# Kernel tuning notes

Hardware: AMD Instinct MI355X
Metric: run time of the kernel (lower is better)

## Reference

```python
import jax, jax.numpy as jnp
import numpy as np

N_NODES = 20000
N_EDGES = 100000
N_SNAP = 2
N_DIM, E_DIM, OUT_DIM, HEADS = 64, 32, 64, 2


def edge_gat(x, ef, src, dst, Wn, We, al, ar, ae, b):
    # DGL EdgeGATConv: fc (no bias), edge-aware attention, edge softmax over
    # incoming edges, message = (ft_src + ft_edge) * alpha, final additive bias.
    H, D = al.shape
    ft = (x @ Wn).reshape(-1, H, D)                # [N,H,D]
    fe = (ef @ We).reshape(-1, H, D)               # [E,H,D]
    el = jnp.einsum('nhd,hd->nh', ft, al)          # [N,H]
    er = jnp.einsum('nhd,hd->nh', ft, ar)          # [N,H]
    ee = jnp.einsum('ehd,hd->eh', fe, ae)          # [E,H]
    logits = jax.nn.leaky_relu(el[src] + er[dst] + ee, 0.2)  # [E,H]
    m = jax.ops.segment_max(logits, dst, num_segments=N_NODES)
    p = jnp.exp(logits - m[dst])
    s = jax.ops.segment_sum(p, dst, num_segments=N_NODES)
    a = p / s[dst]                                 # edge softmax per dst node
    msg = (ft[src] + fe) * a[..., None]            # [E,H,D]
    return jax.ops.segment_sum(msg, dst, num_segments=N_NODES) + b  # [N,H,D]


def gnn_rnn(x, ef, src, dst, params):
    # GNN_RNN.forward per snapshot: stacked EdgeGAT layers, head-mean each.
    for (Wn, We, al, ar, ae, b) in params:
        x = edge_gat(x, ef, src, dst, Wn, We, al, ar, ae, b).mean(axis=1)
    return x


def _mk_layer(key, in_d, e_d, out_d, heads, scale=0.1):
    ks = jax.random.split(key, 6)
    return dict(
        Wn=jax.random.normal(ks[0], (in_d, heads * out_d), jnp.float32) * scale,
        We=jax.random.normal(ks[1], (e_d, heads * out_d), jnp.float32) * scale,
        al=jax.random.normal(ks[2], (heads, out_d), jnp.float32) * scale,
        ar=jax.random.normal(ks[3], (heads, out_d), jnp.float32) * scale,
        ae=jax.random.normal(ks[4], (heads, out_d), jnp.float32) * scale,
        b=jax.random.normal(ks[5], (heads, out_d), jnp.float32) * scale,
    )


def setup_inputs() -> dict:
    key = jax.random.key(0)
    ks = jax.random.split(key, 10)
    inp = {
        'x': jax.random.normal(ks[0], (N_SNAP, N_NODES, N_DIM), jnp.float32),
        'e': jax.random.normal(ks[1], (N_SNAP, N_EDGES, E_DIM), jnp.float32),
        'src': jax.random.randint(ks[2], (N_SNAP, N_EDGES), 0, N_NODES),
        'dst': jax.random.randint(ks[3], (N_SNAP, N_EDGES), 0, N_NODES),
    }
    enc0 = _mk_layer(ks[4], N_DIM, E_DIM, OUT_DIM, HEADS)
    enc1 = _mk_layer(ks[5], OUT_DIM, E_DIM, OUT_DIM, HEADS)
    dec0 = _mk_layer(ks[6], OUT_DIM, E_DIM, N_DIM, HEADS)
    dec1 = _mk_layer(ks[7], N_DIM, E_DIM, N_DIM, HEADS)
    for pref, lp in [('enc0', enc0), ('enc1', enc1), ('dec0', dec0), ('dec1', dec1)]:
        for k, v in lp.items():
            inp[f'{pref}_{k}'] = v
    inp['W_e2d'] = jax.random.normal(ks[8], (OUT_DIM, OUT_DIM), jnp.float32) * 0.1
    return inp


def reference(x, e, src, dst,
              enc0_Wn, enc0_We, enc0_al, enc0_ar, enc0_ae, enc0_b,
              enc1_Wn, enc1_We, enc1_al, enc1_ar, enc1_ae, enc1_b,
              W_e2d,
              dec0_Wn, dec0_We, dec0_al, dec0_ar, dec0_ae, dec0_b,
              dec1_Wn, dec1_We, dec1_al, dec1_ar, dec1_ae, dec1_b):
    enc_params = [(enc0_Wn, enc0_We, enc0_al, enc0_ar, enc0_ae, enc0_b),
                  (enc1_Wn, enc1_We, enc1_al, enc1_ar, enc1_ae, enc1_b)]
    dec_params = [(dec0_Wn, dec0_We, dec0_al, dec0_ar, dec0_ae, dec0_b),
                  (dec1_Wn, dec1_We, dec1_al, dec1_ar, dec1_ae, dec1_b)]

    def per_snapshot(xs, es, ss, ds):
        h = gnn_rnn(xs, es, ss, ds, enc_params)   # encoder, [N,out_dim]
        h = h @ W_e2d.T                           # encoder_to_decoder (no bias)
        return gnn_rnn(h, es, ss, ds, dec_params) # decoder, [N,n_dim]

    decoded = jax.vmap(per_snapshot)(x, e, src, dst)  # [S,N,n_dim]
    return decoded[-1]
```

## Files before the change

kernel.cpp:

```cpp
#include <hip/hip_runtime.h>
#include <math.h>

#define N_NODES 20000
#define N_EDGES 100000

__device__ __forceinline__ float rl_f(float v, int l) {
    return __uint_as_float(__builtin_amdgcn_readlane(__float_as_uint(v), l));
}
__device__ __forceinline__ int rl_i(int v, int l) {
    return __builtin_amdgcn_readlane(v, l);
}
__device__ __forceinline__ float lrelu(float x) { return x > 0.f ? x : 0.2f * x; }

__global__ __launch_bounds__(256) void count_kernel(const int* __restrict__ dst,
                                                    int* __restrict__ cnt,
                                                    int* __restrict__ pos) {
    int e = blockIdx.x * 256 + threadIdx.x;
    if (e < N_EDGES) pos[e] = atomicAdd(&cnt[dst[e]], 1);
}

__global__ __launch_bounds__(256) void scanA_kernel(const int* __restrict__ cnt,
                                                    int* __restrict__ bsum) {
    __shared__ int wsum[4];
    const int tid = threadIdx.x;
    int idx = blockIdx.x * 256 + tid;
    int v = (idx < N_NODES) ? cnt[idx] : 0;
    int s = v;
#pragma unroll
    for (int off = 32; off; off >>= 1) s += __shfl_xor(s, off);
    if ((tid & 63) == 0) wsum[tid >> 6] = s;
    __syncthreads();
    if (tid == 0) bsum[blockIdx.x] = wsum[0] + wsum[1] + wsum[2] + wsum[3];
}

__global__ __launch_bounds__(256) void scanC_kernel(const int* __restrict__ cnt,
                                                    const int* __restrict__ bsum,
                                                    int* __restrict__ row_ptr) {
    __shared__ int sdata[256];
    __shared__ int s_boff;
    const int tid = threadIdx.x;
    const int b = blockIdx.x;
    int idx = b * 256 + tid;
    int v = (idx < N_NODES) ? cnt[idx] : 0;
    sdata[tid] = v;
    if (tid < 64) {
        int a = (tid < b) ? bsum[tid] : 0;
        if (64 + tid < b) a += bsum[64 + tid];
#pragma unroll
        for (int off = 32; off; off >>= 1) a += __shfl_xor(a, off);
        if (tid == 0) s_boff = a;
    }
    __syncthreads();
    for (int off = 1; off < 256; off <<= 1) {
        int t_ = (tid >= off) ? sdata[tid - off] : 0;
        __syncthreads();
        sdata[tid] += t_;
        __syncthreads();
    }
    if (idx < N_NODES) row_ptr[idx] = s_boff + sdata[tid] - v;
    if (b == 0 && tid == 0) row_ptr[N_NODES] = N_EDGES;
}

__global__ __launch_bounds__(256) void permE_kernel(const float* __restrict__ Efeat,
                                                    const int* __restrict__ src,
                                                    const int* __restrict__ dst,
                                                    const int* __restrict__ pos,
                                                    const int* __restrict__ row_ptr,
                                                    float* __restrict__ E_csr,
                                                    int* __restrict__ src_csr) {
    int idx = blockIdx.x * 256 + threadIdx.x;
    int e = idx >> 5, c = idx & 31;
    if (e >= N_EDGES) return;
    int j = row_ptr[dst[e]] + pos[e];
    E_csr[(size_t)j * 32 + c] = Efeat[(size_t)e * 32 + c];
    if (c == 0) src_csr[j] = src[e];
}

__global__ __launch_bounds__(256) void q_kernel(const float* __restrict__ We0, const float* __restrict__ ae0,
                                                const float* __restrict__ We1, const float* __restrict__ ae1,
                                                const float* __restrict__ We2, const float* __restrict__ ae2,
                                                const float* __restrict__ We3, const float* __restrict__ ae3,
                                                float* __restrict__ Q) {
    const int t = threadIdx.x;
    const int k = t >> 3, o = t & 7, L = o >> 1, h = o & 1;
    const float* We = (L == 0) ? We0 : (L == 1) ? We1 : (L == 2) ? We2 : We3;
    const float* ae = (L == 0) ? ae0 : (L == 1) ? ae1 : (L == 2) ? ae2 : ae3;
    float acc = 0.f;
#pragma unroll 8
    for (int d = 0; d < 64; d++) acc = fmaf(We[k * 128 + h * 64 + d], ae[h * 64 + d], acc);
    Q[t] = acc;
}

__global__ __launch_bounds__(256) void ee_kernel(const float* __restrict__ Efeat,
                                                 const int* __restrict__ dst,
                                                 const int* __restrict__ pos,
                                                 const int* __restrict__ row_ptr,
                                                 const float* __restrict__ Q,
                                                 float* __restrict__ EE_csr) {
    __shared__ float QS[256];
    const int tid = threadIdx.x;
    QS[tid] = Q[tid];
    __syncthreads();
    const int e = blockIdx.x * 32 + (tid >> 3);
    const int o = tid & 7;
    if (e >= N_EDGES) return;
    const int j = row_ptr[dst[e]] + pos[e];
    const float4* E4 = (const float4*)(Efeat + (size_t)e * 32);
    float acc = 0.f;
#pragma unroll
    for (int k4 = 0; k4 < 8; k4++) {
        float4 v = E4[k4];
        acc = fmaf(v.x, QS[(k4 * 4 + 0) * 8 + o], acc);
        acc = fmaf(v.y, QS[(k4 * 4 + 1) * 8 + o], acc);
        acc = fmaf(v.z, QS[(k4 * 4 + 2) * 8 + o], acc);
        acc = fmaf(v.w, QS[(k4 * 4 + 3) * 8 + o], acc);
    }
    EE_csr[(size_t)(o >> 1) * 2 * N_EDGES + (size_t)j * 2 + (o & 1)] = acc;
}

__global__ __launch_bounds__(256) void comb_kernel(const float* __restrict__ W_e2d,
                                                   const float* __restrict__ Wn,
                                                   float* __restrict__ Wcomb) {
    int idx = blockIdx.x * 256 + threadIdx.x;
    int j = idx >> 7, c = idx & 127;
    float acc = 0.f;
#pragma unroll 8
    for (int i = 0; i < 64; i++) acc = fmaf(W_e2d[i * 64 + j], Wn[i * 128 + c], acc);
    Wcomb[idx] = acc;
}

__global__ __launch_bounds__(256) void p4_kernel(const float* __restrict__ Wn0, const float* __restrict__ al0, const float* __restrict__ ar0,
                                                 const float* __restrict__ Wn1, const float* __restrict__ al1, const float* __restrict__ ar1,
                                                 const float* __restrict__ Wn2, const float* __restrict__ al2, const float* __restrict__ ar2,
                                                 const float* __restrict__ Wn3, const float* __restrict__ al3, const float* __restrict__ ar3,
                                                 float* __restrict__ P4) {
    const int L = blockIdx.x;
    const float* Wn = (L == 0) ? Wn0 : (L == 1) ? Wn1 : (L == 2) ? Wn2 : Wn3;
    const float* al = (L == 0) ? al0 : (L == 1) ? al1 : (L == 2) ? al2 : al3;
    const float* ar = (L == 0) ? ar0 : (L == 1) ? ar1 : (L == 2) ? ar2 : ar3;
    const int t = threadIdx.x;
    const int k = t >> 2, o = t & 3;
    const float* a = (o & 2) ? ar : al;
    const int h = o & 1;
    float acc = 0.f;
#pragma unroll 8
    for (int d = 0; d < 64; d++) acc = fmaf(Wn[k * 128 + h * 64 + d], a[h * 64 + d], acc);
    P4[L * 256 + t] = acc;
}

__global__ __launch_bounds__(256) void elr_kernel(const float* __restrict__ X,
                                                  const float* __restrict__ P4,
                                                  float2* __restrict__ EL2,
                                                  float2* __restrict__ ER2) {
    const int tid = threadIdx.x;
    const int lane = tid & 63;
    const int wave = tid >> 6;
    const float4 p = ((const float4*)P4)[lane];
    for (int node = blockIdx.x * 4 + wave; node < N_NODES; node += gridDim.x * 4) {
        float xv = X[node * 64 + lane];
        float e0 = xv * p.x, e1 = xv * p.y, f0 = xv * p.z, f1 = xv * p.w;
#pragma unroll
        for (int off = 32; off; off >>= 1) {
            e0 += __shfl_xor(e0, off);
            e1 += __shfl_xor(e1, off);
            f0 += __shfl_xor(f0, off);
            f1 += __shfl_xor(f1, off);
        }
        if (lane == 0) {
            EL2[node] = make_float2(e0, e1);
            ER2[node] = make_float2(f0, f1);
        }
    }
}

__global__ __launch_bounds__(256) void gather_kernel(const float* __restrict__ X,
                                                     const float2* __restrict__ EL2,
                                                     const float2* __restrict__ ER2,
                                                     const float* __restrict__ E_csr,
                                                     const int* __restrict__ src_csr,
                                                     const int* __restrict__ row_ptr,
                                                     const float2* __restrict__ EE_L,
                                                     float2* __restrict__ AX2,
                                                     float* __restrict__ AE) {
    const int tid = threadIdx.x;
    const int lane = tid & 63;
    const int node = blockIdx.x * 4 + (tid >> 6);
    if (node >= N_NODES) return;
    const float NEG_INF = -__builtin_inff();

    const int beg = row_ptr[node], end = row_ptr[node + 1];
    const int deg = end - beg;
    const float2 er = ER2[node];
    float l0 = 0.f, l1 = 0.f, aX0 = 0.f, aX1 = 0.f, aE = 0.f;

    if (deg <= 64) {
        int sn = 0;
        float lg0 = NEG_INF, lg1 = NEG_INF;
        if (lane < deg) {
            sn = src_csr[beg + lane];
            float2 ee = EE_L[beg + lane];
            float2 el = EL2[sn];
            lg0 = lrelu(el.x + er.x + ee.x);
            lg1 = lrelu(el.y + er.y + ee.y);
        }
        float m0 = lg0, m1 = lg1;
#pragma unroll
        for (int off = 32; off; off >>= 1) {
            m0 = fmaxf(m0, __shfl_xor(m0, off));
            m1 = fmaxf(m1, __shfl_xor(m1, off));
        }
        float w0 = (lane < deg) ? __expf(lg0 - m0) : 0.f;
        float w1 = (lane < deg) ? __expf(lg1 - m1) : 0.f;
        l0 = w0;
        l1 = w1;
#pragma unroll
        for (int off = 32; off; off >>= 1) {
            l0 += __shfl_xor(l0, off);
            l1 += __shfl_xor(l1, off);
        }
        int t = 0;
        for (; t + 4 <= deg; t += 4) {
            int s0 = rl_i(sn, t), s1 = rl_i(sn, t + 1);
            int s2 = rl_i(sn, t + 2), s3 = rl_i(sn, t + 3);
            float x0 = X[s0 * 64 + lane];
            float x1 = X[s1 * 64 + lane];
            float x2 = X[s2 * 64 + lane];
            float x3 = X[s3 * 64 + lane];
            const float* Eb = E_csr + (size_t)(beg + t) * 32 + (lane & 31);
            float e0 = Eb[0], e1 = Eb[32], e2 = Eb[64], e3 = Eb[96];
            float w00 = rl_f(w0, t), w01 = rl_f(w0, t + 1);
            float w02 = rl_f(w0, t + 2), w03 = rl_f(w0, t + 3);
            float w10 = rl_f(w1, t), w11 = rl_f(w1, t + 1);
            float w12 = rl_f(w1, t + 2), w13 = rl_f(w1, t + 3);
            aX0 = fmaf(w00, x0, aX0); aX1 = fmaf(w10, x0, aX1);
            aX0 = fmaf(w01, x1, aX0); aX1 = fmaf(w11, x1, aX1);
            aX0 = fmaf(w02, x2, aX0); aX1 = fmaf(w12, x2, aX1);
            aX0 = fmaf(w03, x3, aX0); aX1 = fmaf(w13, x3, aX1);
            aE = fmaf(lane < 32 ? w00 : w10, e0, aE);
            aE = fmaf(lane < 32 ? w01 : w11, e1, aE);
            aE = fmaf(lane < 32 ? w02 : w12, e2, aE);
            aE = fmaf(lane < 32 ? w03 : w13, e3, aE);
        }
        for (; t < deg; t++) {
            int st = rl_i(sn, t);
            float w0t = rl_f(w0, t), w1t = rl_f(w1, t);
            float xv = X[st * 64 + lane];
            float ev = E_csr[(size_t)(beg + t) * 32 + (lane & 31)];
            aX0 = fmaf(w0t, xv, aX0);
            aX1 = fmaf(w1t, xv, aX1);
            aE = fmaf(lane < 32 ? w0t : w1t, ev, aE);
        }
    } else {
        float m0 = NEG_INF, m1 = NEG_INF;
        for (int c = beg; c < end; c += 64) {
            int j = c + lane;
            float lg0 = NEG_INF, lg1 = NEG_INF;
            if (j < end) {
                int sn_ = src_csr[j];
                float2 ee = EE_L[j];
                float2 el = EL2[sn_];
                lg0 = lrelu(el.x + er.x + ee.x);
                lg1 = lrelu(el.y + er.y + ee.y);
            }
#pragma unroll
            for (int off = 32; off; off >>= 1) {
                lg0 = fmaxf(lg0, __shfl_xor(lg0, off));
                lg1 = fmaxf(lg1, __shfl_xor(lg1, off));
            }
            m0 = fmaxf(m0, lg0);
            m1 = fmaxf(m1, lg1);
        }
        for (int c = beg; c < end; c += 64) {
            int j = c + lane;
            int sn_ = 0;
            float lg0 = NEG_INF, lg1 = NEG_INF;
            if (j < end) {
                sn_ = src_csr[j];
                float2 ee = EE_L[j];
                float2 el = EL2[sn_];
                lg0 = lrelu(el.x + er.x + ee.x);
                lg1 = lrelu(el.y + er.y + ee.y);
            }
            float w0c = (j < end) ? __expf(lg0 - m0) : 0.f;
            float w1c = (j < end) ? __expf(lg1 - m1) : 0.f;
            float s0 = w0c, s1 = w1c;
#pragma unroll
            for (int off = 32; off; off >>= 1) {
                s0 += __shfl_xor(s0, off);
                s1 += __shfl_xor(s1, off);
            }
            l0 += s0;
            l1 += s1;
            int nch = (end - c) < 64 ? (end - c) : 64;
            for (int t = 0; t < nch; t++) {
                int st = rl_i(sn_, t);
                float w0t = rl_f(w0c, t), w1t = rl_f(w1c, t);
                float xv = X[st * 64 + lane];
                float ev = E_csr[(size_t)(c + t) * 32 + (lane & 31)];
                aX0 = fmaf(w0t, xv, aX0);
                aX1 = fmaf(w1t, xv, aX1);
                aE = fmaf(lane < 32 ? w0t : w1t, ev, aE);
            }
        }
    }
    const float inv0 = l0 > 0.f ? 1.f / l0 : 0.f;
    const float inv1 = l1 > 0.f ? 1.f / l1 : 0.f;
    AX2[node * 64 + lane] = make_float2(aX0 * inv0, aX1 * inv1);
    AE[node * 64 + lane] = aE * (lane < 32 ? inv0 : inv1);
}

__global__ __launch_bounds__(256) void epilogue_kernel(const float2* __restrict__ AX2,
                                                       const float* __restrict__ AE,
                                                       const float* __restrict__ Wn,
                                                       const float* __restrict__ We,
                                                       const float* __restrict__ bias,
                                                       const float* __restrict__ P4next,
                                                       const int has_next,
                                                       float* __restrict__ OUT,
                                                       float2* __restrict__ EL2,
                                                       float2* __restrict__ ER2) {
    __shared__ float4 WnS4[32 * 64];
    __shared__ float4 WeS4[16 * 64];
    const int tid = threadIdx.x;
    for (int idx = tid; idx < 32 * 64; idx += 256) {
        int k2 = idx >> 6, l = idx & 63;
        WnS4[idx] = make_float4(Wn[(2 * k2) * 128 + l], Wn[(2 * k2) * 128 + 64 + l],
                                Wn[(2 * k2 + 1) * 128 + l], Wn[(2 * k2 + 1) * 128 + 64 + l]);
    }
    for (int idx = tid; idx < 16 * 64; idx += 256) {
        int k2 = idx >> 6, l = idx & 63;
        WeS4[idx] = make_float4(We[(2 * k2) * 128 + l], We[(2 * k2) * 128 + 64 + l],
                                We[(2 * k2 + 1) * 128 + l], We[(2 * k2 + 1) * 128 + 64 + l]);
    }
    __syncthreads();
    const int lane = tid & 63;
    const int wave = tid >> 6;
    const float b0 = bias[lane], b1 = bias[64 + lane];
    const float4 p = has_next ? ((const float4*)P4next)[lane] : make_float4(0.f, 0.f, 0.f, 0.f);

    for (int base = blockIdx.x * 8 + wave * 2; base < N_NODES; base += gridDim.x * 8) {
        const int n0 = base, n1 = base + 1;
        float2 axa = AX2[n0 * 64 + lane];
        float2 axb = AX2[n1 * 64 + lane];
        float aea = AE[n0 * 64 + lane];
        float aeb = AE[n1 * 64 + lane];
        float r0a = 0.f, r1a = 0.f, r0b = 0.f, r1b = 0.f;
#pragma unroll
        for (int k2 = 0; k2 < 32; k2++) {
            float4 w4 = WnS4[k2 * 64 + lane];
            float a00 = rl_f(axa.x, 2 * k2), a01 = rl_f(axa.x, 2 * k2 + 1);
            float a10 = rl_f(axa.y, 2 * k2), a11 = rl_f(axa.y, 2 * k2 + 1);
            float c00 = rl_f(axb.x, 2 * k2), c01 = rl_f(axb.x, 2 * k2 + 1);
            float c10 = rl_f(axb.y, 2 * k2), c11 = rl_f(axb.y, 2 * k2 + 1);
            r0a = fmaf(a00, w4.x, r0a); r1a = fmaf(a10, w4.y, r1a);
            r0a = fmaf(a01, w4.z, r0a); r1a = fmaf(a11, w4.w, r1a);
            r0b = fmaf(c00, w4.x, r0b); r1b = fmaf(c10, w4.y, r1b);
            r0b = fmaf(c01, w4.z, r0b); r1b = fmaf(c11, w4.w, r1b);
        }
#pragma unroll
        for (int k2 = 0; k2 < 16; k2++) {
            float4 w4 = WeS4[k2 * 64 + lane];
            float a00 = rl_f(aea, 2 * k2), a01 = rl_f(aea, 2 * k2 + 1);
            float a10 = rl_f(aea, 32 + 2 * k2), a11 = rl_f(aea, 32 + 2 * k2 + 1);
            float c00 = rl_f(aeb, 2 * k2), c01 = rl_f(aeb, 2 * k2 + 1);
            float c10 = rl_f(aeb, 32 + 2 * k2), c11 = rl_f(aeb, 32 + 2 * k2 + 1);
            r0a = fmaf(a00, w4.x, r0a); r1a = fmaf(a10, w4.y, r1a);
            r0a = fmaf(a01, w4.z, r0a); r1a = fmaf(a11, w4.w, r1a);
            r0b = fmaf(c00, w4.x, r0b); r1b = fmaf(c10, w4.y, r1b);
            r0b = fmaf(c01, w4.z, r0b); r1b = fmaf(c11, w4.w, r1b);
        }
        float outa = 0.5f * (r0a + b0 + r1a + b1);
        float outb = 0.5f * (r0b + b0 + r1b + b1);
        OUT[n0 * 64 + lane] = outa;
        OUT[n1 * 64 + lane] = outb;
        if (has_next) {
            float e0a = outa * p.x, e1a = outa * p.y, f0a = outa * p.z, f1a = outa * p.w;
            float e0b = outb * p.x, e1b = outb * p.y, f0b = outb * p.z, f1b = outb * p.w;
#pragma unroll
            for (int off = 32; off; off >>= 1) {
                e0a += __shfl_xor(e0a, off); e1a += __shfl_xor(e1a, off);
                f0a += __shfl_xor(f0a, off); f1a += __shfl_xor(f1a, off);
                e0b += __shfl_xor(e0b, off); e1b += __shfl_xor(e1b, off);
                f0b += __shfl_xor(f0b, off); f1b += __shfl_xor(f1b, off);
            }
            if (lane == 0) {
                EL2[n0] = make_float2(e0a, e1a);
                ER2[n0] = make_float2(f0a, f1a);
                EL2[n1] = make_float2(e0b, e1b);
                ER2[n1] = make_float2(f0b, f1b);
            }
        }
    }
}

extern "C" void kernel_launch(void* const* d_in, const int* in_sizes, int n_in,
                              void* d_out, int out_size, void* d_ws, size_t ws_size,
                              hipStream_t stream) {
    const float* x = (const float*)d_in[0];
    const float* e = (const float*)d_in[1];
    const int* src = (const int*)d_in[2];
    const int* dst = (const int*)d_in[3];

    const float* x1 = x + (size_t)1 * N_NODES * 64;
    const float* e1 = e + (size_t)1 * N_EDGES * 32;
    const int* src1 = src + N_EDGES;
    const int* dst1 = dst + N_EDGES;

    int we2d_idx, dec0_b, dec1_b;
    if (in_sizes[16] == 64 * 64 && in_sizes[17] == 64 * 128) {
        we2d_idx = 16; dec0_b = 17; dec1_b = 23;
    } else {
        dec0_b = 16; dec1_b = 22; we2d_idx = 28;
    }
    auto P = [&](int i) { return (const float*)d_in[i]; };

    char* ws = (char*)d_ws;
    int* cnt      = (int*)(ws + 0);
    int* row_ptr  = (int*)(ws + 80000);
    int* pos      = (int*)(ws + 160064);
    int* bsum     = (int*)(ws + 560064);
    float* q      = (float*)(ws + 560576);
    int* src_csr  = (int*)(ws + 561600);
    float* e_csr  = (float*)(ws + 961600);
    float* ee_csr = (float*)(ws + 13761600);
    float* p4_all = (float*)(ws + 16961600);
    float* el     = (float*)(ws + 16965696);
    float* er     = (float*)(ws + 17125696);
    float* ax     = (float*)(ws + 17285696);
    float* ae     = (float*)(ws + 27525696);
    float* h      = (float*)(ws + 32645696);
    float* wcomb  = (float*)(ws + 37765696);

    hipMemsetAsync(cnt, 0, N_NODES * sizeof(int), stream);
    const int EB = (N_EDGES + 255) / 256;
    const int SB = (N_NODES + 255) / 256;
    count_kernel<<<EB, 256, 0, stream>>>(dst1, cnt, pos);
    scanA_kernel<<<SB, 256, 0, stream>>>(cnt, bsum);
    scanC_kernel<<<SB, 256, 0, stream>>>(cnt, bsum, row_ptr);

    permE_kernel<<<(N_EDGES * 32) / 256, 256, 0, stream>>>(e1, src1, dst1, pos,
                                                           row_ptr, e_csr, src_csr);
    q_kernel<<<1, 256, 0, stream>>>(P(5), P(8), P(11), P(14),
                                    P(dec0_b + 1), P(dec0_b + 4),
                                    P(dec1_b + 1), P(dec1_b + 4), q);
    ee_kernel<<<(N_EDGES + 31) / 32, 256, 0, stream>>>(e1, dst1, pos, row_ptr, q, ee_csr);
    comb_kernel<<<32, 256, 0, stream>>>(P(we2d_idx), P(dec0_b + 0), wcomb);
    p4_kernel<<<4, 256, 0, stream>>>(P(4), P(6), P(7),
                                     P(10), P(12), P(13),
                                     wcomb, P(dec0_b + 2), P(dec0_b + 3),
                                     P(dec1_b + 0), P(dec1_b + 2), P(dec1_b + 3),
                                     p4_all);
    elr_kernel<<<1280, 256, 0, stream>>>(x1, p4_all, (float2*)el, (float2*)er);

    const int NB_G = (N_NODES + 3) / 4;
    const int NB_E = 768;

    auto run_layer = [&](const float* Xin, const float* Wn, const float* We_,
                         const float* b_, int L, float* Out) {
        gather_kernel<<<NB_G, 256, 0, stream>>>(
            Xin, (const float2*)el, (const float2*)er, e_csr, src_csr, row_ptr,
            (const float2*)(ee_csr) + (size_t)L * N_EDGES, (float2*)ax, ae);
        epilogue_kernel<<<NB_E, 256, 0, stream>>>(
            (const float2*)ax, ae, Wn, We_, b_, p4_all + (L + 1) * 256, (L < 3) ? 1 : 0,
            Out, (float2*)el, (float2*)er);
    };

    run_layer(x1, P(4), P(5), P(9), 0, h);
    run_layer(h, P(10), P(11), P(15), 1, h);
    run_layer(h, wcomb, P(dec0_b + 1), P(dec0_b + 5), 2, h);
    run_layer(h, P(dec1_b + 0), P(dec1_b + 1), P(dec1_b + 5), 3, (float*)d_out);
}
```

Measured before the change: 332.0 us.

## Fuse setup kernels and process two nodes per wavefront in gather

Merges the parameter-prep kernels (P4, Wcomb, Q, el/er) into one multi-role launch and fuses edge permutation with edge-attention scoring into a single prep kernel. The gather kernel now handles two destination nodes per wavefront, using half-waves for the softmax when both degrees are at most 32, with a per-node fallback path for larger degrees. Epilogue grid size also changes. The aim is fewer launches and better lane utilization for low-degree nodes, at the cost of a serialized two-node accumulation loop and more branching.

New measurement: 354.0 us. +6.7%, slower.

```diff
diff --git a/kernel.cpp b/kernel.cpp
--- a/kernel.cpp
+++ b/kernel.cpp
@@ -61,116 +61,137 @@
     if (b == 0 && tid == 0) row_ptr[N_NODES] = N_EDGES;
 }
 
-__global__ __launch_bounds__(256) void permE_kernel(const float* __restrict__ Efeat,
-                                                    const int* __restrict__ src,
-                                                    const int* __restrict__ dst,
-                                                    const int* __restrict__ pos,
-                                                    const int* __restrict__ row_ptr,
-                                                    float* __restrict__ E_csr,
-                                                    int* __restrict__ src_csr) {
-    int idx = blockIdx.x * 256 + threadIdx.x;
-    int e = idx >> 5, c = idx & 31;
-    if (e >= N_EDGES) return;
-    int j = row_ptr[dst[e]] + pos[e];
-    E_csr[(size_t)j * 32 + c] = Efeat[(size_t)e * 32 + c];
-    if (c == 0) src_csr[j] = src[e];
-}
-
-__global__ __launch_bounds__(256) void q_kernel(const float* __restrict__ We0, const float* __restrict__ ae0,
-                                                const float* __restrict__ We1, const float* __restrict__ ae1,
-                                                const float* __restrict__ We2, const float* __restrict__ ae2,
-                                                const float* __restrict__ We3, const float* __restrict__ ae3,
-                                                float* __restrict__ Q) {
+__global__ __launch_bounds__(256) void params_kernel(
+    const float* __restrict__ Wn0, const float* __restrict__ al0, const float* __restrict__ ar0,
+    const float* __restrict__ Wn1, const float* __restrict__ al1, const float* __restrict__ ar1,
+    const float* __restrict__ dWn, const float* __restrict__ al2, const float* __restrict__ ar2,
+    const float* __restrict__ Wn3, const float* __restrict__ al3, const float* __restrict__ ar3,
+    const float* __restrict__ W_e2d,
+    const float* __restrict__ We0, const float* __restrict__ ae0,
+    const float* __restrict__ We1, const float* __restrict__ ae1,
+    const float* __restrict__ We2, const float* __restrict__ ae2,
+    const float* __restrict__ We3, const float* __restrict__ ae3,
+    const float* __restrict__ X0,
+    float* __restrict__ P4, float* __restrict__ Wcomb, float* __restrict__ Q,
+    float2* __restrict__ EL2, float2* __restrict__ ER2) {
+    __shared__ float praw[256];
+    const int b = blockIdx.x;
     const int t = threadIdx.x;
-    const int k = t >> 3, o = t & 7, L = o >> 1, h = o & 1;
-    const float* We = (L == 0) ? We0 : (L == 1) ? We1 : (L == 2) ? We2 : We3;
-    const float* ae = (L == 0) ? ae0 : (L == 1) ? ae1 : (L == 2) ? ae2 : ae3;
-    float acc = 0.f;
+
+    if (b < 4) {
+        const int L = b;
+        if (L != 2) {
+            const float* Wn = (L == 0) ? Wn0 : (L == 1) ? Wn1 : Wn3;
+            const float* al = (L == 0) ? al0 : (L == 1) ? al1 : al3;
+            const float* ar = (L == 0) ? ar0 : (L == 1) ? ar1 : ar3;
+            const int k = t >> 2, o = t & 3;
+            const float* a = (o & 2) ? ar : al;
+            const int h = o & 1;
+            float acc = 0.f;
 #pragma unroll 8
-    for (int d = 0; d < 64; d++) acc = fmaf(We[k * 128 + h * 64 + d], ae[h * 64 + d], acc);
-    Q[t] = acc;
-}
-
-__global__ __launch_bounds__(256) void ee_kernel(const float* __restrict__ Efeat,
-                                                 const int* __restrict__ dst,
-                                                 const int* __restrict__ pos,
-                                                 const int* __restrict__ row_ptr,
-                                                 const float* __restrict__ Q,
-                                                 float* __restrict__ EE_csr) {
+            for (int d = 0; d < 64; d++) acc = fmaf(Wn[k * 128 + h * 64 + d], a[h * 64 + d], acc);
+            P4[L * 256 + t] = acc;
+        } else {
+            {
+                const int i = t >> 2, o = t & 3;
+                const float* a = (o & 2) ? ar2 : al2;
+                const int h = o & 1;
+                float acc = 0.f;
+#pragma unroll 8
+                for (int d = 0; d < 64; d++) acc = fmaf(dWn[i * 128 + h * 64 + d], a[h * 64 + d], acc);
+                praw[t] = acc;
+            }
+            __syncthreads();
+            const int j = t >> 2, o = t & 3;
+            float acc = 0.f;
+#pragma unroll 8
+            for (int i = 0; i < 64; i++) acc = fmaf(W_e2d[i * 64 + j], praw[i * 4 + o], acc);
+            P4[2 * 256 + t] = acc;
+        }
+    } else if (b < 36) {
+        int idx = (b - 4) * 256 + t;
+        int j = idx >> 7, c = idx & 127;
+        float acc = 0.f;
+#pragma unroll 8
+        for (int i = 0; i < 64; i++) acc = fmaf(W_e2d[i * 64 + j], dWn[i * 128 + c], acc);
+        Wcomb[idx] = acc;
+    } else if (b == 36) {
+        const int k = t >> 3, o = t & 7, L = o >> 1, h = o & 1;
+        const float* We = (L == 0) ? We0 : (L == 1) ? We1 : (L == 2) ? We2 : We3;
+        const float* ae = (L == 0) ? ae0 : (L == 1) ? ae1 : (L == 2) ? ae2 : ae3;
+        float acc = 0.f;
+#pragma unroll 8
+        for (int d = 0; d < 64; d++) acc = fmaf(We[k * 128 + h * 64 + d], ae[h * 64 + d], acc);
+        Q[t] = acc;
+    } else {
+        {
+            const int k = t >> 2, o = t & 3;
+            const float* a = (o & 2) ? ar0 : al0;
+            const int h = o & 1;
+            float acc = 0.f;
+#pragma unroll 8
+            for (int d = 0; d < 64; d++) acc = fmaf(Wn0[k * 128 + h * 64 + d], a[h * 64 + d], acc);
+            praw[t] = acc;
+        }
+        __syncthreads();
+        const int lane = t & 63;
+        const int wave = t >> 6;
+        const float px = praw[lane * 4 + 0], py = praw[lane * 4 + 1];
+        const float pz = praw[lane * 4 + 2], pw = praw[lane * 4 + 3];
+        const int nb = gridDim.x - 37;
+        for (int node = (b - 37) * 4 + wave; node < N_NODES; node += nb * 4) {
+            float xv = X0[node * 64 + lane];
+            float e0 = xv * px, e1 = xv * py, f0 = xv * pz, f1 = xv * pw;
+#pragma unroll
+            for (int off = 32; off; off >>= 1) {
+                e0 += __shfl_xor(e0, off);
+                e1 += __shfl_xor(e1, off);
+                f0 += __shfl_xor(f0, off);
+                f1 += __shfl_xor(f1, off);
+            }
+            if (lane == 0) {
+                EL2[node] = make_float2(e0, e1);
+                ER2[node] = make_float2(f0, f1);
+            }
+        }
+    }
+}
+
+__global__ __launch_bounds__(256) void prep_kernel(const float* __restrict__ Efeat,
+                                                   const int* __restrict__ src,
+                                                   const int* __restrict__ dst,
+                                                   const int* __restrict__ pos,
+                                                   const int* __restrict__ row_ptr,
+                                                   const float* __restrict__ Q,
+                                                   float* __restrict__ E_csr,
+                                                   int* __restrict__ src_csr,
+                                                   float* __restrict__ EE_csr) {
     __shared__ float QS[256];
+    __shared__ float ES[32][33];
+    __shared__ int JS[32];
     const int tid = threadIdx.x;
     QS[tid] = Q[tid];
+    const int e0 = blockIdx.x * 32;
+    const int el_ = tid >> 3, quad = tid & 7;
+    float4 v = ((const float4*)Efeat)[(size_t)(e0 + el_) * 8 + quad];
+    ES[el_][quad * 4 + 0] = v.x;
+    ES[el_][quad * 4 + 1] = v.y;
+    ES[el_][quad * 4 + 2] = v.z;
+    ES[el_][quad * 4 + 3] = v.w;
+    if (tid < 32) {
+        int e = e0 + tid;
+        int j = row_ptr[dst[e]] + pos[e];
+        JS[tid] = j;
+        src_csr[j] = src[e];
+    }
     __syncthreads();
-    const int e = blockIdx.x * 32 + (tid >> 3);
-    const int o = tid & 7;
-    if (e >= N_EDGES) return;
-    const int j = row_ptr[dst[e]] + pos[e];
-    const float4* E4 = (const float4*)(Efeat + (size_t)e * 32);
+    const int j = JS[el_];
+    ((float4*)E_csr)[(size_t)j * 8 + quad] = v;
+    const int o = quad;
     float acc = 0.f;
 #pragma unroll
-    for (int k4 = 0; k4 < 8; k4++) {
-        float4 v = E4[k4];
-        acc = fmaf(v.x, QS[(k4 * 4 + 0) * 8 + o], acc);
-        acc = fmaf(v.y, QS[(k4 * 4 + 1) * 8 + o], acc);
-        acc = fmaf(v.z, QS[(k4 * 4 + 2) * 8 + o], acc);
-        acc = fmaf(v.w, QS[(k4 * 4 + 3) * 8 + o], acc);
-    }
+    for (int k = 0; k < 32; k++) acc = fmaf(ES[el_][k], QS[k * 8 + o], acc);
     EE_csr[(size_t)(o >> 1) * 2 * N_EDGES + (size_t)j * 2 + (o & 1)] = acc;
-}
-
-__global__ __launch_bounds__(256) void comb_kernel(const float* __restrict__ W_e2d,
-                                                   const float* __restrict__ Wn,
-                                                   float* __restrict__ Wcomb) {
-    int idx = blockIdx.x * 256 + threadIdx.x;
-    int j = idx >> 7, c = idx & 127;
-    float acc = 0.f;
-#pragma unroll 8
-    for (int i = 0; i < 64; i++) acc = fmaf(W_e2d[i * 64 + j], Wn[i * 128 + c], acc);
-    Wcomb[idx] = acc;
-}
-
-__global__ __launch_bounds__(256) void p4_kernel(const float* __restrict__ Wn0, const float* __restrict__ al0, const float* __restrict__ ar0,
-                                                 const float* __restrict__ Wn1, const float* __restrict__ al1, const float* __restrict__ ar1,
-                                                 const float* __restrict__ Wn2, const float* __restrict__ al2, const float* __restrict__ ar2,
-                                                 const float* __restrict__ Wn3, const float* __restrict__ al3, const float* __restrict__ ar3,
-                                                 float* __restrict__ P4) {
-    const int L = blockIdx.x;
-    const float* Wn = (L == 0) ? Wn0 : (L == 1) ? Wn1 : (L == 2) ? Wn2 : Wn3;
-    const float* al = (L == 0) ? al0 : (L == 1) ? al1 : (L == 2) ? al2 : al3;
-    const float* ar = (L == 0) ? ar0 : (L == 1) ? ar1 : (L == 2) ? ar2 : ar3;
-    const int t = threadIdx.x;
-    const int k = t >> 2, o = t & 3;
-    const float* a = (o & 2) ? ar : al;
-    const int h = o & 1;
-    float acc = 0.f;
-#pragma unroll 8
-    for (int d = 0; d < 64; d++) acc = fmaf(Wn[k * 128 + h * 64 + d], a[h * 64 + d], acc);
-    P4[L * 256 + t] = acc;
-}
-
-__global__ __launch_bounds__(256) void elr_kernel(const float* __restrict__ X,
-                                                  const float* __restrict__ P4,
-                                                  float2* __restrict__ EL2,
-                                                  float2* __restrict__ ER2) {
-    const int tid = threadIdx.x;
-    const int lane = tid & 63;
-    const int wave = tid >> 6;
-    const float4 p = ((const float4*)P4)[lane];
-    for (int node = blockIdx.x * 4 + wave; node < N_NODES; node += gridDim.x * 4) {
-        float xv = X[node * 64 + lane];
-        float e0 = xv * p.x, e1 = xv * p.y, f0 = xv * p.z, f1 = xv * p.w;
-#pragma unroll
-        for (int off = 32; off; off >>= 1) {
-            e0 += __shfl_xor(e0, off);
-            e1 += __shfl_xor(e1, off);
-            f0 += __shfl_xor(f0, off);
-            f1 += __shfl_xor(f1, off);
-        }
-        if (lane == 0) {
-            EL2[node] = make_float2(e0, e1);
-            ER2[node] = make_float2(f0, f1);
-        }
-    }
 }
 
 __global__ __launch_bounds__(256) void gather_kernel(const float* __restrict__ X,
@@ -184,129 +205,143 @@
                                                      float* __restrict__ AE) {
     const int tid = threadIdx.x;
     const int lane = tid & 63;
-    const int node = blockIdx.x * 4 + (tid >> 6);
-    if (node >= N_NODES) return;
+    const int pair = blockIdx.x * 4 + (tid >> 6);
+    const int nA = pair * 2;
+    if (nA >= N_NODES) return;
+    const int nB = nA + 1;
+    const int half = lane >> 5, hl = lane & 31;
+    const int begA = row_ptr[nA];
+    const int begB = row_ptr[nB];
+    const int endB = row_ptr[nB + 1];
+    const int degA = begB - begA, degB = endB - begB;
     const float NEG_INF = -__builtin_inff();
 
-    const int beg = row_ptr[node], end = row_ptr[node + 1];
-    const int deg = end - beg;
-    const float2 er = ER2[node];
-    float l0 = 0.f, l1 = 0.f, aX0 = 0.f, aX1 = 0.f, aE = 0.f;
-
-    if (deg <= 64) {
+    if (degA <= 32 && degB <= 32) {
+        const float2 erA = ER2[nA], erB = ER2[nB];
+        const int myBeg = half ? begB : begA;
+        const int myDeg = half ? degB : degA;
+        const float erx = half ? erB.x : erA.x;
+        const float ery = half ? erB.y : erA.y;
         int sn = 0;
         float lg0 = NEG_INF, lg1 = NEG_INF;
-        if (lane < deg) {
-            sn = src_csr[beg + lane];
-            float2 ee = EE_L[beg + lane];
+        if (hl < myDeg) {
+            int j = myBeg + hl;
+            sn = src_csr[j];
+            float2 ee = EE_L[j];
             float2 el = EL2[sn];
-            lg0 = lrelu(el.x + er.x + ee.x);
-            lg1 = lrelu(el.y + er.y + ee.y);
+            lg0 = lrelu(el.x + erx + ee.x);
+            lg1 = lrelu(el.y + ery + ee.y);
         }
         float m0 = lg0, m1 = lg1;
 #pragma unroll
-        for (int off = 32; off; off >>= 1) {
+        for (int off = 16; off; off >>= 1) {
             m0 = fmaxf(m0, __shfl_xor(m0, off));
             m1 = fmaxf(m1, __shfl_xor(m1, off));
         }
-        float w0 = (lane < deg) ? __expf(lg0 - m0) : 0.f;
-        float w1 = (lane < deg) ? __expf(lg1 - m1) : 0.f;
-        l0 = w0;
-        l1 = w1;
-#pragma unroll
-        for (int off = 32; off; off >>= 1) {
+        float w0 = (hl < myDeg) ? __expf(lg0 - m0) : 0.f;
+        float w1 = (hl < myDeg) ? __expf(lg1 - m1) : 0.f;
+        float l0 = w0, l1 = w1;
+#pragma unroll
+        for (int off = 16; off; off >>= 1) {
             l0 += __shfl_xor(l0, off);
             l1 += __shfl_xor(l1, off);
         }
-        int t = 0;
-        for (; t + 4 <= deg; t += 4) {
-            int s0 = rl_i(sn, t), s1 = rl_i(sn, t + 1);
-            int s2 = rl_i(sn, t + 2), s3 = rl_i(sn, t + 3);
-            float x0 = X[s0 * 64 + lane];
-            float x1 = X[s1 * 64 + lane];
-            float x2 = X[s2 * 64 + lane];
-            float x3 = X[s3 * 64 + lane];
-            const float* Eb = E_csr + (size_t)(beg + t) * 32 + (lane & 31);
-            float e0 = Eb[0], e1 = Eb[32], e2 = Eb[64], e3 = Eb[96];
-            float w00 = rl_f(w0, t), w01 = rl_f(w0, t + 1);
-            float w02 = rl_f(w0, t + 2), w03 = rl_f(w0, t + 3);
-            float w10 = rl_f(w1, t), w11 = rl_f(w1, t + 1);
-            float w12 = rl_f(w1, t + 2), w13 = rl_f(w1, t + 3);
-            aX0 = fmaf(w00, x0, aX0); aX1 = fmaf(w10, x0, aX1);
-            aX0 = fmaf(w01, x1, aX0); aX1 = fmaf(w11, x1, aX1);
-            aX0 = fmaf(w02, x2, aX0); aX1 = fmaf(w12, x2, aX1);
-            aX0 = fmaf(w03, x3, aX0); aX1 = fmaf(w13, x3, aX1);
-            aE = fmaf(lane < 32 ? w00 : w10, e0, aE);
-            aE = fmaf(lane < 32 ? w01 : w11, e1, aE);
-            aE = fmaf(lane < 32 ? w02 : w12, e2, aE);
-            aE = fmaf(lane < 32 ? w03 : w13, e3, aE);
-        }
-        for (; t < deg; t++) {
-            int st = rl_i(sn, t);
-            float w0t = rl_f(w0, t), w1t = rl_f(w1, t);
-            float xv = X[st * 64 + lane];
-            float ev = E_csr[(size_t)(beg + t) * 32 + (lane & 31)];
-            aX0 = fmaf(w0t, xv, aX0);
-            aX1 = fmaf(w1t, xv, aX1);
-            aE = fmaf(lane < 32 ? w0t : w1t, ev, aE);
-        }
+        float lA0 = rl_f(l0, 0), lA1 = rl_f(l1, 0);
+        float lB0 = rl_f(l0, 32), lB1 = rl_f(l1, 32);
+        float iA0 = lA0 > 0.f ? 1.f / lA0 : 0.f;
+        float iA1 = lA1 > 0.f ? 1.f / lA1 : 0.f;
+        float iB0 = lB0 > 0.f ? 1.f / lB0 : 0.f;
+        float iB1 = lB1 > 0.f ? 1.f / lB1 : 0.f;
+
+        float aXA0 = 0.f, aXA1 = 0.f, aXB0 = 0.f, aXB1 = 0.f, aEA = 0.f, aEB = 0.f;
+        const int dmax = degA > degB ? degA : degB;
+        for (int t = 0; t < dmax; t++) {
+            if (t < degA) {
+                int s = rl_i(sn, t);
+                float wa0 = rl_f(w0, t), wa1 = rl_f(w1, t);
+                float xv = X[s * 64 + lane];
+                float ev = E_csr[(size_t)(begA + t) * 32 + hl];
+                aXA0 = fmaf(wa0, xv, aXA0);
+                aXA1 = fmaf(wa1, xv, aXA1);
+                aEA = fmaf(half ? wa1 : wa0, ev, aEA);
+            }
+            if (t < degB) {
+                int s = rl_i(sn, 32 + t);
+                float wb0 = rl_f(w0, 32 + t), wb1 = rl_f(w1, 32 + t);
+                float xv = X[s * 64 + lane];
+                float ev = E_csr[(size_t)(begB + t) * 32 + hl];
+                aXB0 = fmaf(wb0, xv, aXB0);
+                aXB1 = fmaf(wb1, xv, aXB1);
+                aEB = fmaf(half ? wb1 : wb0, ev, aEB);
+            }
+        }
+        AX2[nA * 64 + lane] = make_float2(aXA0 * iA0, aXA1 * iA1);
+        AX2[nB * 64 + lane] = make_float2(aXB0 * iB0, aXB1 * iB1);
+        AE[nA * 64 + lane] = aEA * (half ? iA1 : iA0);
+        AE[nB * 64 + lane] = aEB * (half ? iB1 : iB0);
     } else {
-        float m0 = NEG_INF, m1 = NEG_INF;
-        for (int c = beg; c < end; c += 64) {
-            int j = c + lane;
-            float lg0 = NEG_INF, lg1 = NEG_INF;
-            if (j < end) {
-                int sn_ = src_csr[j];
-                float2 ee = EE_L[j];
-                float2 el = EL2[sn_];
-                lg0 = lrelu(el.x + er.x + ee.x);
-                lg1 = lrelu(el.y + er.y + ee.y);
-            }
-#pragma unroll
-            for (int off = 32; off; off >>= 1) {
-                lg0 = fmaxf(lg0, __shfl_xor(lg0, off));
-                lg1 = fmaxf(lg1, __shfl_xor(lg1, off));
-            }
-            m0 = fmaxf(m0, lg0);
-            m1 = fmaxf(m1, lg1);
-        }
-        for (int c = beg; c < end; c += 64) {
-            int j = c + lane;
-            int sn_ = 0;
-            float lg0 = NEG_INF, lg1 = NEG_INF;
-            if (j < end) {
-                sn_ = src_csr[j];
-                float2 ee = EE_L[j];
-                float2 el = EL2[sn_];
-                lg0 = lrelu(el.x + er.x + ee.x);
-                lg1 = lrelu(el.y + er.y + ee.y);
-            }
-            float w0c = (j < end) ? __expf(lg0 - m0) : 0.f;
-            float w1c = (j < end) ? __expf(lg1 - m1) : 0.f;
-            float s0 = w0c, s1 = w1c;
-#pragma unroll
-            for (int off = 32; off; off >>= 1) {
-                s0 += __shfl_xor(s0, off);
-                s1 += __shfl_xor(s1, off);
-            }
-            l0 += s0;
-            l1 += s1;
-            int nch = (end - c) < 64 ? (end - c) : 64;
-            for (int t = 0; t < nch; t++) {
-                int st = rl_i(sn_, t);
-                float w0t = rl_f(w0c, t), w1t = rl_f(w1c, t);
-                float xv = X[st * 64 + lane];
-                float ev = E_csr[(size_t)(c + t) * 32 + (lane & 31)];
-                aX0 = fmaf(w0t, xv, aX0);
-                aX1 = fmaf(w1t, xv, aX1);
-                aE = fmaf(lane < 32 ? w0t : w1t, ev, aE);
-            }
-        }
-    }
-    const float inv0 = l0 > 0.f ? 1.f / l0 : 0.f;
-    const float inv1 = l1 > 0.f ? 1.f / l1 : 0.f;
-    AX2[node * 64 + lane] = make_float2(aX0 * inv0, aX1 * inv1);
-    AE[node * 64 + lane] = aE * (lane < 32 ? inv0 : inv1);
+        for (int node = nA; node <= nB; node++) {
+            const int beg = (node == nA) ? begA : begB;
+            const int end = (node == nA) ? begB : endB;
+            const float2 er = ER2[node];
+            float m0 = NEG_INF, m1 = NEG_INF;
+            for (int c = beg; c < end; c += 64) {
+                int j = c + lane;
+                float lg0 = NEG_INF, lg1 = NEG_INF;
+                if (j < end) {
+                    int sn_ = src_csr[j];
+                    float2 ee = EE_L[j];
+                    float2 el = EL2[sn_];
+                    lg0 = lrelu(el.x + er.x + ee.x);
+                    lg1 = lrelu(el.y + er.y + ee.y);
+                }
+#pragma unroll
+                for (int off = 32; off; off >>= 1) {
+                    lg0 = fmaxf(lg0, __shfl_xor(lg0, off));
+                    lg1 = fmaxf(lg1, __shfl_xor(lg1, off));
+                }
+                m0 = fmaxf(m0, lg0);
+                m1 = fmaxf(m1, lg1);
+            }
+            float l0 = 0.f, l1 = 0.f, aX0 = 0.f, aX1 = 0.f, aE = 0.f;
+            for (int c = beg; c < end; c += 64) {
+                int j = c + lane;
+                int sn_ = 0;
+                float lg0 = NEG_INF, lg1 = NEG_INF;
+                if (j < end) {
+                    sn_ = src_csr[j];
+                    float2 ee = EE_L[j];
+                    float2 el = EL2[sn_];
+                    lg0 = lrelu(el.x + er.x + ee.x);
+                    lg1 = lrelu(el.y + er.y + ee.y);
+                }
+                float w0c = (j < end) ? __expf(lg0 - m0) : 0.f;
+                float w1c = (j < end) ? __expf(lg1 - m1) : 0.f;
+                float s0 = w0c, s1 = w1c;
+#pragma unroll
+                for (int off = 32; off; off >>= 1) {
+                    s0 += __shfl_xor(s0, off);
+                    s1 += __shfl_xor(s1, off);
+                }
+                l0 += s0;
+                l1 += s1;
+                int nch = (end - c) < 64 ? (end - c) : 64;
+                for (int t = 0; t < nch; t++) {
+                    int st = rl_i(sn_, t);
+                    float w0t = rl_f(w0c, t), w1t = rl_f(w1c, t);
+                    float xv = X[st * 64 + lane];
+                    float ev = E_csr[(size_t)(c + t) * 32 + hl];
+                    aX0 = fmaf(w0t, xv, aX0);
+                    aX1 = fmaf(w1t, xv, aX1);
+                    aE = fmaf(half ? w1t : w0t, ev, aE);
+                }
+            }
+            const float inv0 = l0 > 0.f ? 1.f / l0 : 0.f;
+            const float inv1 = l1 > 0.f ? 1.f / l1 : 0.f;
+            AX2[node * 64 + lane] = make_float2(aX0 * inv0, aX1 * inv1);
+            AE[node * 64 + lane] = aE * (half ? inv1 : inv0);
+        }
+    }
 }
 
 __global__ __launch_bounds__(256) void epilogue_kernel(const float2* __restrict__ AX2,
@@ -438,22 +473,22 @@
     scanA_kernel<<<SB, 256, 0, stream>>>(cnt, bsum);
     scanC_kernel<<<SB, 256, 0, stream>>>(cnt, bsum, row_ptr);
 
-    permE_kernel<<<(N_EDGES * 32) / 256, 256, 0, stream>>>(e1, src1, dst1, pos,
-                                                           row_ptr, e_csr, src_csr);
-    q_kernel<<<1, 256, 0, stream>>>(P(5), P(8), P(11), P(14),
-                                    P(dec0_b + 1), P(dec0_b + 4),
-                                    P(dec1_b + 1), P(dec1_b + 4), q);
-    ee_kernel<<<(N_EDGES + 31) / 32, 256, 0, stream>>>(e1, dst1, pos, row_ptr, q, ee_csr);
-    comb_kernel<<<32, 256, 0, stream>>>(P(we2d_idx), P(dec0_b + 0), wcomb);
-    p4_kernel<<<4, 256, 0, stream>>>(P(4), P(6), P(7),
-                                     P(10), P(12), P(13),
-                                     wcomb, P(dec0_b + 2), P(dec0_b + 3),
-                                     P(dec1_b + 0), P(dec1_b + 2), P(dec1_b + 3),
-                                     p4_all);
-    elr_kernel<<<1280, 256, 0, stream>>>(x1, p4_all, (float2*)el, (float2*)er);
-
-    const int NB_G = (N_NODES + 3) / 4;
-    const int NB_E = 768;
+    params_kernel<<<512, 256, 0, stream>>>(
+        P(4), P(6), P(7),
+        P(10), P(12), P(13),
+        P(dec0_b + 0), P(dec0_b + 2), P(dec0_b + 3),
+        P(dec1_b + 0), P(dec1_b + 2), P(dec1_b + 3),
+        P(we2d_idx),
+        P(5), P(8), P(11), P(14),
+        P(dec0_b + 1), P(dec0_b + 4), P(dec1_b + 1), P(dec1_b + 4),
+        x1,
+        p4_all, wcomb, q, (float2*)el, (float2*)er);
+
+    prep_kernel<<<N_EDGES / 32, 256, 0, stream>>>(e1, src1, dst1, pos, row_ptr, q,
+                                                  e_csr, src_csr, ee_csr);
+
+    const int NB_G = N_NODES / 8;
+    const int NB_E = 625;
 
     auto run_layer = [&](const float* Xin, const float* Wn, const float* We_,
                          const float* b_, int L, float* Out) {
```
